# Kernel optimization log

Hardware: AMD Instinct MI355X
Metric: run time of the kernel (lower is better)

Reference implementation:

```python
import jax, jax.numpy as jnp
import numpy as np

NEG_SLOPE = 0.2
BN_EPS = 1e-5

def lrelu(x):
    return jnp.where(x >= 0, x, NEG_SLOPE * x)

def setup_inputs() -> dict:
    key = jax.random.key(0)
    ks = jax.random.split(key, 12)
    B, V, D = 256, 16, 512
    s = lambda fan_in: 1.0 / np.sqrt(fan_in)
    return {
        "F": jax.random.normal(ks[0], (B, V, D), dtype=jnp.float32),
        # Relation MLP: Linear(1024,512) x3 (stored as (in,out))
        "W1": jax.random.uniform(ks[1], (2 * D, D), jnp.float32, -s(2 * D), s(2 * D)),
        "b1": jax.random.uniform(ks[2], (D,), jnp.float32, -s(2 * D), s(2 * D)),
        "W2": jax.random.uniform(ks[3], (D, D), jnp.float32, -s(D), s(D)),
        "b2": jax.random.uniform(ks[4], (D,), jnp.float32, -s(D), s(D)),
        "W3": jax.random.uniform(ks[5], (D, D), jnp.float32, -s(D), s(D)),
        "b3": jax.random.uniform(ks[6], (D,), jnp.float32, -s(D), s(D)),
        # Fusion: Linear(1024,512) + BatchNorm1d(512)
        "Wf": jax.random.uniform(ks[7], (2 * D, D), jnp.float32, -s(2 * D), s(2 * D)),
        "bf": jax.random.uniform(ks[8], (D,), jnp.float32, -s(2 * D), s(2 * D)),
        "gamma": jnp.ones((D,), jnp.float32),
        "beta": jnp.zeros((D,), jnp.float32),
    }

def reference(F, W1, b1, W2, b2, W3, b3, Wf, bf, gamma, beta):
    B, V, D = F.shape
    # All-pairs broadcast + concat -> (B, V, V, 2D)
    F_i = jnp.broadcast_to(F[:, :, None, :], (B, V, V, D))
    F_j = jnp.broadcast_to(F[:, None, :, :], (B, V, V, D))
    M = jnp.concatenate([F_i, F_j], axis=-1)
    # 3-layer Relation MLP with LeakyReLU(0.2)
    h = lrelu(M @ W1 + b1)
    h = lrelu(h @ W2 + b2)
    h = lrelu(h @ W3 + b3)
    # Sum over neighbor axis (dim -2) -> (B, V, D)
    Msum = jnp.sum(h, axis=-2)
    # Fusion: concat, Linear, BatchNorm1d (training-mode batch stats), LeakyReLU
    X = jnp.concatenate([F, Msum], axis=-1).reshape(-1, 2 * D)  # (B*V, 2D)
    y = X @ Wf + bf
    mean = jnp.mean(y, axis=0)
    var = jnp.mean(jnp.square(y - mean), axis=0)  # biased var (torch BN)
    yn = (y - mean) * jax.lax.rsqrt(var + BN_EPS) * gamma + beta
    return lrelu(yn).reshape(B, V, D)
```

## Files before the change

kernel.cpp:

```cpp
#include <hip/hip_runtime.h>

using f32x4  = __attribute__((ext_vector_type(4))) float;
using bf16x8 = __attribute__((ext_vector_type(8))) __bf16;

static constexpr int DD = 512;
static constexpr int NTOK = 4096;

__device__ __forceinline__ float bf2f(unsigned short u) {
  unsigned int v = ((unsigned int)u) << 16;
  return __builtin_bit_cast(float, v);
}
__device__ __forceinline__ float bflo(unsigned int u) {
  return __builtin_bit_cast(float, u << 16);
}
__device__ __forceinline__ float bfhi(unsigned int u) {
  return __builtin_bit_cast(float, u & 0xffff0000u);
}
__device__ __forceinline__ unsigned short f2bf(float f) {
  unsigned int u = __builtin_bit_cast(unsigned int, f);
  unsigned int r = u + 0x7fffu + ((u >> 16) & 1u);
  return (unsigned short)(r >> 16);
}
__device__ __forceinline__ float lrelu(float v) { return v >= 0.f ? v : 0.2f * v; }


__global__ __launch_bounds__(256) void k_prep(const float* __restrict__ F,
                                              const float* __restrict__ W1,
                                              const float* __restrict__ W2,
                                              const float* __restrict__ W3,
                                              const float* __restrict__ Wf,
                                              unsigned short* __restrict__ XP,
                                              unsigned short* __restrict__ W1P,
                                              unsigned short* __restrict__ W2P,
                                              unsigned short* __restrict__ W3P,
                                              unsigned short* __restrict__ WfP,
                                              float* __restrict__ sums) {
  const int bid = blockIdx.x, tid = threadIdx.x;
  if (bid < 8192) {
    int idx = (bid << 8) + tid;
    int t = idx >> 9, c = idx & 511;
    XP[((t >> 4) * 32 + (c >> 5)) * 512 + ((c >> 3) & 3) * 128 + (t & 15) * 8 + (c & 7)] = f2bf(F[idx]);
  } else if (bid < 10240) {
    int idx = ((bid - 8192) << 8) + tid;
    int k = idx >> 10, n = idx & 1023;
    float v = W1[(n < 512 ? k : 512 + k) * 512 + (n & 511)];
    W1P[((n >> 4) * 16 + (k >> 5)) * 512 + ((k >> 3) & 3) * 128 + (n & 15) * 8 + (k & 7)] = f2bf(v);
  } else if (bid < 11264) {
    int idx = ((bid - 10240) << 8) + tid;
    int k = idx >> 9, n = idx & 511;
    int off = (((n >> 6) * 16 + (k >> 5)) * 4 + ((n >> 4) & 3)) * 512 + ((k >> 3) & 3) * 128 + (n & 15) * 8 + (k & 7);
    W2P[off] = f2bf(W2[idx]);
  } else if (bid < 12288) {
    int idx = ((bid - 11264) << 8) + tid;
    int k = idx >> 9, n = idx & 511;
    int off = (((n >> 6) * 16 + (k >> 5)) * 4 + ((n >> 4) & 3)) * 512 + ((k >> 3) & 3) * 128 + (n & 15) * 8 + (k & 7);
    W3P[off] = f2bf(W3[idx]);
  } else if (bid < 14336) {
    int idx = ((bid - 12288) << 8) + tid;
    int k = idx >> 9, n = idx & 511;
    WfP[((n >> 4) * 32 + (k >> 5)) * 512 + ((k >> 3) & 3) * 128 + (n & 15) * 8 + (k & 7)] = f2bf(Wf[idx]);
  } else {
    reinterpret_cast<float4*>(sums)[tid] = float4{0.f, 0.f, 0.f, 0.f};
  }
}

__global__ __launch_bounds__(512) void k_gemm_ac(const unsigned short* __restrict__ XP,
                                                 const unsigned short* __restrict__ W1P,
                                                 unsigned short* __restrict__ ACP) {
  const int tid = threadIdx.x, lane = tid & 63, wid = tid >> 6;
  const int wm = wid >> 2, wn = wid & 3;
  const int l15 = lane & 15;
  const int bx = blockIdx.x, by = blockIdx.y;

  f32x4 acc[2][4];
#pragma unroll
  for (int mt = 0; mt < 2; ++mt)
#pragma unroll
    for (int nt = 0; nt < 4; ++nt) acc[mt][nt] = f32x4{0.f, 0.f, 0.f, 0.f};

  bf16x8 ca[2], cb[4], na[2], nb[4];
  auto ldA = [&](bf16x8 (&d)[2], int ks) {
#pragma unroll
    for (int mt = 0; mt < 2; ++mt)
      d[mt] = *reinterpret_cast<const bf16x8*>(XP + (((bx * 4 + wm * 2 + mt) * 32 + ks) << 9) + lane * 8);
  };
  auto ldB = [&](bf16x8 (&d)[4], int ks) {
#pragma unroll
    for (int nt = 0; nt < 4; ++nt)
      d[nt] = *reinterpret_cast<const bf16x8*>(W1P + ((((by * 16 + wn * 4 + nt) * 16) + ks) << 9) + lane * 8);
  };

  ldA(ca, 0); ldB(cb, 0);
  for (int ks = 0; ks < 16; ++ks) {
    int kn = (ks + 1) & 15;
    ldA(na, kn); ldB(nb, kn);
    __builtin_amdgcn_s_setprio(1);
#pragma unroll
    for (int mt = 0; mt < 2; ++mt)
#pragma unroll
      for (int nt = 0; nt < 4; ++nt)
        acc[mt][nt] = __builtin_amdgcn_mfma_f32_16x16x32_bf16(ca[mt], cb[nt], acc[mt][nt], 0, 0, 0);
    __builtin_amdgcn_s_setprio(0);
#pragma unroll
    for (int q = 0; q < 2; ++q) ca[q] = na[q];
#pragma unroll
    for (int q = 0; q < 4; ++q) cb[q] = nb[q];
  }
#pragma unroll
  for (int mt = 0; mt < 2; ++mt)
#pragma unroll
    for (int nt = 0; nt < 4; ++nt) {
      int col = by * 256 + wn * 64 + nt * 16 + l15;
      int panel = bx * 4 + wm * 2 + mt;
#pragma unroll
      for (int r = 0; r < 4; ++r) {
        int rowi = (lane >> 4) * 4 + r;
        ACP[(panel * 32 + (col >> 5)) * 512 + ((col >> 3) & 3) * 128 + rowi * 8 + (col & 7)] = f2bf(acc[mt][nt][r]);
      }
    }
}

__global__ __launch_bounds__(1024) void k_relation(const unsigned short* __restrict__ ACP,
                                                   const unsigned short* __restrict__ W2P,
                                                   const unsigned short* __restrict__ W3P,
                                                   const float* __restrict__ b1,
                                                   const float* __restrict__ b2,
                                                   const float* __restrict__ b3,
                                                   unsigned short* __restrict__ XP) {
  __shared__ unsigned short lds[65536];
  char* ldsb = reinterpret_cast<char*>(lds);
  const int tid = threadIdx.x;
  const int b = blockIdx.x >> 1, half = blockIdx.x & 1;

  {
    const int r = tid >> 3;
    const int kh = (tid >> 2) & 1;
    const int kq = tid & 3;
    const int il = r >> 4, j = r & 15;
    const int rowA = half * 8 + il;
#pragma unroll
    for (int kk = 0; kk < 8; ++kk) {
      const int ks = kh * 8 + kk;
      const int c = ks * 32 + kq * 8;
      uint4 av = *reinterpret_cast<const uint4*>(ACP + ((b * 32 + ks) << 9) + kq * 128 + rowA * 8);
      uint4 cv = *reinterpret_cast<const uint4*>(ACP + ((b * 32 + 16 + ks) << 9) + kq * 128 + j * 8);
      float4 bv0 = *reinterpret_cast<const float4*>(b1 + c);
      float4 bv1 = *reinterpret_cast<const float4*>(b1 + c + 4);
      unsigned int au[4] = {av.x, av.y, av.z, av.w};
      unsigned int cu[4] = {cv.x, cv.y, cv.z, cv.w};
      float bb[8] = {bv0.x, bv0.y, bv0.z, bv0.w, bv1.x, bv1.y, bv1.z, bv1.w};
      unsigned int ou[4];
#pragma unroll
      for (int q = 0; q < 4; ++q) {
        float v0 = lrelu(bflo(au[q]) + bflo(cu[q]) + bb[2 * q]);
        float v1 = lrelu(bfhi(au[q]) + bfhi(cu[q]) + bb[2 * q + 1]);
        ou[q] = ((unsigned int)f2bf(v1) << 16) | (unsigned int)f2bf(v0);
      }
      uint4 o; o.x = ou[0]; o.y = ou[1]; o.z = ou[2]; o.w = ou[3];
      *reinterpret_cast<uint4*>(ldsb + ((r >> 4) * 16 + ks) * 1024 + kq * 256 + (r & 15) * 16) = o;
    }
  }
  __syncthreads();

  const int lane = tid & 63, wid = tid >> 6;
  const int l15 = lane & 15;
  const int fg = wid >> 1;
  const int rg = wid & 1;

  const unsigned short* w2base = W2P + (fg << 15) + lane * 8;
  const unsigned short* w3base = W3P + (fg << 15) + lane * 8;
  const char* lrd = ldsb + rg * 65536 + lane * 16;
  char* lwr = ldsb + rg * 65536 + fg * 2048 + ((lane >> 5) & 1) * 256 + ((lane >> 4) & 1) * 8 + l15 * 16;

  f32x4 acc[4][4];
  bf16x8 a[2][4], cb[4];

  auto layer = [&](const unsigned short* __restrict__ wb) {
#pragma unroll
    for (int mt = 0; mt < 4; ++mt)
#pragma unroll
      for (int nt = 0; nt < 4; ++nt) acc[mt][nt] = f32x4{0.f, 0.f, 0.f, 0.f};
#pragma unroll
    for (int mt = 0; mt < 4; ++mt)
      a[0][mt] = *reinterpret_cast<const bf16x8*>(wb + mt * 512);
#pragma unroll
    for (int ks = 0; ks < 16; ++ks) {
      const int cur = ks & 1, nxt = cur ^ 1;
      const int ksn = (ks + 1) & 15;
#pragma unroll
      for (int mt = 0; mt < 4; ++mt)
        a[nxt][mt] = *reinterpret_cast<const bf16x8*>(wb + ksn * 2048 + mt * 512);
#pragma unroll
      for (int nt = 0; nt < 4; ++nt)
        cb[nt] = *reinterpret_cast<const bf16x8*>(lrd + nt * 16384 + ks * 1024);
      __builtin_amdgcn_s_setprio(1);
#pragma unroll
      for (int mt = 0; mt < 4; ++mt)
#pragma unroll
        for (int nt = 0; nt < 4; ++nt)
          acc[mt][nt] = __builtin_amdgcn_mfma_f32_16x16x32_bf16(a[cur][mt], cb[nt], acc[mt][nt], 0, 0, 0);
      __builtin_amdgcn_s_setprio(0);
    }
  };

  auto store_h = [&](const float* __restrict__ bias) {
#pragma unroll
    for (int mt = 0; mt < 4; ++mt) {
      float4 bv = *reinterpret_cast<const float4*>(bias + fg * 64 + mt * 16 + ((lane >> 4) & 3) * 4);
#pragma unroll
      for (int nt = 0; nt < 4; ++nt) {
        unsigned int w0 = f2bf(lrelu(acc[mt][nt][0] + bv.x));
        unsigned int w1 = f2bf(lrelu(acc[mt][nt][1] + bv.y));
        unsigned int w2 = f2bf(lrelu(acc[mt][nt][2] + bv.z));
        unsigned int w3 = f2bf(lrelu(acc[mt][nt][3] + bv.w));
        uint2 val; val.x = (w1 << 16) | w0; val.y = (w3 << 16) | w2;
        *reinterpret_cast<uint2*>(lwr + nt * 16384 + (mt >> 1) * 1024 + (mt & 1) * 512) = val;
      }
    }
  };

  layer(w2base);
  __syncthreads();
  store_h(b2);
  __syncthreads();
  layer(w3base);
  __syncthreads();
  store_h(b3);
  __syncthreads();

  if (wid < 8) {
    const int t = wid;
    const int ks = lane >> 2, kq = lane & 3;
    const char* base = ldsb + (t * 16 + ks) * 1024 + kq * 256;
    float s[8] = {0.f, 0.f, 0.f, 0.f, 0.f, 0.f, 0.f, 0.f};
#pragma unroll
    for (int it = 0; it < 16; ++it) {
      int j = (it + lane + (lane >> 3)) & 15;
      uint4 v = *reinterpret_cast<const uint4*>(base + j * 16);
      s[0] += bflo(v.x); s[1] += bfhi(v.x);
      s[2] += bflo(v.y); s[3] += bfhi(v.y);
      s[4] += bflo(v.z); s[5] += bfhi(v.z);
      s[6] += bflo(v.w); s[7] += bfhi(v.w);
    }
    uint4 o;
    o.x = ((unsigned int)f2bf(s[1]) << 16) | f2bf(s[0]);
    o.y = ((unsigned int)f2bf(s[3]) << 16) | f2bf(s[2]);
    o.z = ((unsigned int)f2bf(s[5]) << 16) | f2bf(s[4]);
    o.w = ((unsigned int)f2bf(s[7]) << 16) | f2bf(s[6]);
    int tg15 = half * 8 + t;
    *reinterpret_cast<uint4*>(XP + ((b * 32 + 16 + ks) << 9) + kq * 128 + tg15 * 8) = o;
  }
}

__global__ __launch_bounds__(512) void k_fusion(const unsigned short* __restrict__ XP,
                                                const unsigned short* __restrict__ WfP,
                                                const float* __restrict__ bfv,
                                                float* __restrict__ y,
                                                float* __restrict__ sums,
                                                float* __restrict__ sumsq) {
  const int tid = threadIdx.x, lane = tid & 63, wid = tid >> 6;
  const int wm = wid >> 2, wn = wid & 3;
  const int l15 = lane & 15;
  const int bx = blockIdx.x, by = blockIdx.y;
  const int rowbase = bx * 64 + wm * 32;
  const int colbase = by * 128 + wn * 32;

  f32x4 acc[2][2];
#pragma unroll
  for (int mt = 0; mt < 2; ++mt)
#pragma unroll
    for (int nt = 0; nt < 2; ++nt) acc[mt][nt] = f32x4{0.f, 0.f, 0.f, 0.f};

  bf16x8 ca[2], cb[2], na[2], nb[2];
  auto ldA = [&](bf16x8 (&d)[2], int ks) {
#pragma unroll
    for (int mt = 0; mt < 2; ++mt)
      d[mt] = *reinterpret_cast<const bf16x8*>(XP + (((bx * 4 + wm * 2 + mt) * 32 + ks) << 9) + lane * 8);
  };
  auto ldB = [&](bf16x8 (&d)[2], int ks) {
#pragma unroll
    for (int nt = 0; nt < 2; ++nt)
      d[nt] = *reinterpret_cast<const bf16x8*>(WfP + (((by * 8 + wn * 2 + nt) * 32 + ks) << 9) + lane * 8);
  };

  ldA(ca, 0); ldB(cb, 0);
  for (int ks = 0; ks < 32; ++ks) {
    int kn = (ks + 1) & 31;
    ldA(na, kn); ldB(nb, kn);
    __builtin_amdgcn_s_setprio(1);
#pragma unroll
    for (int mt = 0; mt < 2; ++mt)
#pragma unroll
      for (int nt = 0; nt < 2; ++nt)
        acc[mt][nt] = __builtin_amdgcn_mfma_f32_16x16x32_bf16(ca[mt], cb[nt], acc[mt][nt], 0, 0, 0);
    __builtin_amdgcn_s_setprio(0);
#pragma unroll
    for (int q = 0; q < 2; ++q) { ca[q] = na[q]; cb[q] = nb[q]; }
  }

  float s[2] = {0.f, 0.f}, q2[2] = {0.f, 0.f};
#pragma unroll
  for (int nt = 0; nt < 2; ++nt) {
    int col = colbase + nt * 16 + l15;
    float bias = bfv[col];
#pragma unroll
    for (int mt = 0; mt < 2; ++mt)
#pragma unroll
      for (int r = 0; r < 4; ++r) {
        int row = rowbase + mt * 16 + (lane >> 4) * 4 + r;
        float v = acc[mt][nt][r] + bias;
        y[row * DD + col] = v;
        s[nt] += v; q2[nt] += v * v;
      }
  }
#pragma unroll
  for (int nt = 0; nt < 2; ++nt) {
    s[nt] += __shfl_xor(s[nt], 16);  s[nt] += __shfl_xor(s[nt], 32);
    q2[nt] += __shfl_xor(q2[nt], 16); q2[nt] += __shfl_xor(q2[nt], 32);
    if (lane < 16) {
      int col = colbase + nt * 16 + l15;
      atomicAdd(&sums[col], s[nt]);
      atomicAdd(&sumsq[col], q2[nt]);
    }
  }
}

__global__ __launch_bounds__(256) void k_bnapply(const float* __restrict__ y,
                                                 const float* __restrict__ sums,
                                                 const float* __restrict__ sumsq,
                                                 const float* __restrict__ gamma,
                                                 const float* __restrict__ beta,
                                                 float* __restrict__ out) {
  int idx = blockIdx.x * 256 + threadIdx.x;
  if (idx >= NTOK * DD) return;
  int c = idx & 511;
  float mean = sums[c] * (1.0f / 4096.0f);
  float var = sumsq[c] * (1.0f / 4096.0f) - mean * mean;
  float rstd = rsqrtf(var + 1e-5f);
  float v = (y[idx] - mean) * rstd * gamma[c] + beta[c];
  out[idx] = lrelu(v);
}

extern "C" void kernel_launch(void* const* d_in, const int* in_sizes, int n_in,
                              void* d_out, int out_size, void* d_ws, size_t ws_size,
                              hipStream_t stream) {
  const float* F   = (const float*)d_in[0];
  const float* W1  = (const float*)d_in[1];
  const float* b1  = (const float*)d_in[2];
  const float* W2  = (const float*)d_in[3];
  const float* b2  = (const float*)d_in[4];
  const float* W3  = (const float*)d_in[5];
  const float* b3  = (const float*)d_in[6];
  const float* Wf  = (const float*)d_in[7];
  const float* bfv = (const float*)d_in[8];
  const float* gamma = (const float*)d_in[9];
  const float* beta  = (const float*)d_in[10];
  float* out = (float*)d_out;

  char* ws = (char*)d_ws;
  unsigned short* XP  = (unsigned short*)(ws);
  unsigned short* ACP = (unsigned short*)(ws + (8u << 20));
  unsigned short* W1P = (unsigned short*)(ws + (16u << 20));
  unsigned short* W2P = (unsigned short*)(ws + (17u << 20));
  unsigned short* W3P = (unsigned short*)(ws + (17u << 20) + (512u << 10));
  unsigned short* WfP = (unsigned short*)(ws + (18u << 20));
  float* y            = (float*)(ws + (19u << 20));
  float* sums         = (float*)(ws + (27u << 20));
  float* sumsq        = sums + 512;

  k_prep<<<14337, 256, 0, stream>>>(F, W1, W2, W3, Wf, XP, W1P, W2P, W3P, WfP, sums);
  k_gemm_ac<<<dim3(64, 4), 512, 0, stream>>>(XP, W1P, ACP);
  k_relation<<<512, 1024, 0, stream>>>(ACP, W2P, W3P, b1, b2, b3, XP);
  k_fusion<<<dim3(64, 4), 512, 0, stream>>>(XP, WfP, bfv, y, sums, sumsq);
  k_bnapply<<<(NTOK * DD + 255) / 256, 256, 0, stream>>>(y, sums, sumsq, gamma, beta, out);
}
```

Baseline: 124.3 us.

## Switch relation MLP to 32x32x16 MFMA with matching weight and LDS layouts

Replaces the 4x4 grid of 16x16x32 bf16 MFMAs in the relation kernel with a 2x2 grid of 32x32x16 MFMAs per wave. The W2/W3 packing, the LDS layout for the hidden activations, the layer-1 staging and the neighbor-sum readout are all re-indexed to fit the new fragment shapes. The k-loop is now a rolled, software-pipelined ping-pong over 32 k-steps, and launch_bounds gains a minimum-occupancy hint. The aim is fewer fragment loads per FLOP and fewer MFMA issues, at the cost of new LDS bank-conflict patterns and a possible register-pressure cap from the occupancy hint.

```diff
diff --git a/kernel.cpp b/kernel.cpp
--- a/kernel.cpp
+++ b/kernel.cpp
@@ -1,6 +1,7 @@
 #include <hip/hip_runtime.h>
 
 using f32x4  = __attribute__((ext_vector_type(4))) float;
+using f32x16 = __attribute__((ext_vector_type(16))) float;
 using bf16x8 = __attribute__((ext_vector_type(8))) __bf16;
 
 static constexpr int DD = 512;
@@ -48,12 +49,14 @@
   } else if (bid < 11264) {
     int idx = ((bid - 10240) << 8) + tid;
     int k = idx >> 9, n = idx & 511;
-    int off = (((n >> 6) * 16 + (k >> 5)) * 4 + ((n >> 4) & 3)) * 512 + ((k >> 3) & 3) * 128 + (n & 15) * 8 + (k & 7);
+    int off = (((n >> 6) * 32 + (k >> 4)) * 2 + ((n >> 5) & 1)) * 512 +
+              ((k >> 3) & 1) * 256 + (n & 31) * 8 + (k & 7);
     W2P[off] = f2bf(W2[idx]);
   } else if (bid < 12288) {
     int idx = ((bid - 11264) << 8) + tid;
     int k = idx >> 9, n = idx & 511;
-    int off = (((n >> 6) * 16 + (k >> 5)) * 4 + ((n >> 4) & 3)) * 512 + ((k >> 3) & 3) * 128 + (n & 15) * 8 + (k & 7);
+    int off = (((n >> 6) * 32 + (k >> 4)) * 2 + ((n >> 5) & 1)) * 512 +
+              ((k >> 3) & 1) * 256 + (n & 31) * 8 + (k & 7);
     W3P[off] = f2bf(W3[idx]);
   } else if (bid < 14336) {
     int idx = ((bid - 12288) << 8) + tid;
@@ -120,32 +123,31 @@
     }
 }
 
-__global__ __launch_bounds__(1024) void k_relation(const unsigned short* __restrict__ ACP,
-                                                   const unsigned short* __restrict__ W2P,
-                                                   const unsigned short* __restrict__ W3P,
-                                                   const float* __restrict__ b1,
-                                                   const float* __restrict__ b2,
-                                                   const float* __restrict__ b3,
-                                                   unsigned short* __restrict__ XP) {
+__global__ __launch_bounds__(1024, 4) void k_relation(const unsigned short* __restrict__ ACP,
+                                                      const unsigned short* __restrict__ W2P,
+                                                      const unsigned short* __restrict__ W3P,
+                                                      const float* __restrict__ b1,
+                                                      const float* __restrict__ b2,
+                                                      const float* __restrict__ b3,
+                                                      unsigned short* __restrict__ XP) {
   __shared__ unsigned short lds[65536];
   char* ldsb = reinterpret_cast<char*>(lds);
   const int tid = threadIdx.x;
   const int b = blockIdx.x >> 1, half = blockIdx.x & 1;
 
   {
-    const int r = tid >> 3;
-    const int kh = (tid >> 2) & 1;
-    const int kq = tid & 3;
+    const int c8b = (tid >> 3) & 7;
+    const int r = ((tid >> 6) << 3) | (tid & 7);
     const int il = r >> 4, j = r & 15;
     const int rowA = half * 8 + il;
-#pragma unroll
-    for (int kk = 0; kk < 8; ++kk) {
-      const int ks = kh * 8 + kk;
-      const int c = ks * 32 + kq * 8;
-      uint4 av = *reinterpret_cast<const uint4*>(ACP + ((b * 32 + ks) << 9) + kq * 128 + rowA * 8);
-      uint4 cv = *reinterpret_cast<const uint4*>(ACP + ((b * 32 + 16 + ks) << 9) + kq * 128 + j * 8);
-      float4 bv0 = *reinterpret_cast<const float4*>(b1 + c);
-      float4 bv1 = *reinterpret_cast<const float4*>(b1 + c + 4);
+    const int rt = r >> 5, r31 = r & 31;
+#pragma unroll
+    for (int it = 0; it < 8; ++it) {
+      const int c8 = c8b + it * 8;
+      uint4 av = *reinterpret_cast<const uint4*>(ACP + ((b * 32 + (c8 >> 2)) << 9) + (c8 & 3) * 128 + rowA * 8);
+      uint4 cv = *reinterpret_cast<const uint4*>(ACP + ((b * 32 + 16 + (c8 >> 2)) << 9) + (c8 & 3) * 128 + j * 8);
+      float4 bv0 = *reinterpret_cast<const float4*>(b1 + c8 * 8);
+      float4 bv1 = *reinterpret_cast<const float4*>(b1 + c8 * 8 + 4);
       unsigned int au[4] = {av.x, av.y, av.z, av.w};
       unsigned int cu[4] = {cv.x, cv.y, cv.z, cv.w};
       float bb[8] = {bv0.x, bv0.y, bv0.z, bv0.w, bv1.x, bv1.y, bv1.z, bv1.w};
@@ -157,66 +159,78 @@
         ou[q] = ((unsigned int)f2bf(v1) << 16) | (unsigned int)f2bf(v0);
       }
       uint4 o; o.x = ou[0]; o.y = ou[1]; o.z = ou[2]; o.w = ou[3];
-      *reinterpret_cast<uint4*>(ldsb + ((r >> 4) * 16 + ks) * 1024 + kq * 256 + (r & 15) * 16) = o;
+      *reinterpret_cast<uint4*>(ldsb + (rt * 32 + (c8 >> 1)) * 1024 + (c8 & 1) * 512 + r31 * 16) = o;
     }
   }
   __syncthreads();
 
   const int lane = tid & 63, wid = tid >> 6;
-  const int l15 = lane & 15;
+  const int r31 = lane & 31, h = lane >> 5;
   const int fg = wid >> 1;
   const int rg = wid & 1;
 
   const unsigned short* w2base = W2P + (fg << 15) + lane * 8;
   const unsigned short* w3base = W3P + (fg << 15) + lane * 8;
-  const char* lrd = ldsb + rg * 65536 + lane * 16;
-  char* lwr = ldsb + rg * 65536 + fg * 2048 + ((lane >> 5) & 1) * 256 + ((lane >> 4) & 1) * 8 + l15 * 16;
-
-  f32x4 acc[4][4];
-  bf16x8 a[2][4], cb[4];
+  const unsigned short* lrd = lds + (rg * 2) * 32 * 512 + lane * 8;
+
+  f32x16 acc[2][2];
+  bf16x8 aA[2], aB[2], bA[2], bB[2];
+
+  auto ldA_ = [&](bf16x8 (&d)[2], const unsigned short* __restrict__ wb, int ks) {
+    d[0] = *reinterpret_cast<const bf16x8*>(wb + ks * 1024);
+    d[1] = *reinterpret_cast<const bf16x8*>(wb + ks * 1024 + 512);
+  };
+  auto ldB_ = [&](bf16x8 (&d)[2], int ks) {
+    d[0] = *reinterpret_cast<const bf16x8*>(lrd + ks * 512);
+    d[1] = *reinterpret_cast<const bf16x8*>(lrd + 32 * 512 + ks * 512);
+  };
 
   auto layer = [&](const unsigned short* __restrict__ wb) {
 #pragma unroll
-    for (int mt = 0; mt < 4; ++mt)
-#pragma unroll
-      for (int nt = 0; nt < 4; ++nt) acc[mt][nt] = f32x4{0.f, 0.f, 0.f, 0.f};
-#pragma unroll
-    for (int mt = 0; mt < 4; ++mt)
-      a[0][mt] = *reinterpret_cast<const bf16x8*>(wb + mt * 512);
-#pragma unroll
-    for (int ks = 0; ks < 16; ++ks) {
-      const int cur = ks & 1, nxt = cur ^ 1;
-      const int ksn = (ks + 1) & 15;
-#pragma unroll
-      for (int mt = 0; mt < 4; ++mt)
-        a[nxt][mt] = *reinterpret_cast<const bf16x8*>(wb + ksn * 2048 + mt * 512);
-#pragma unroll
-      for (int nt = 0; nt < 4; ++nt)
-        cb[nt] = *reinterpret_cast<const bf16x8*>(lrd + nt * 16384 + ks * 1024);
+    for (int mt = 0; mt < 2; ++mt)
+#pragma unroll
+      for (int nt = 0; nt < 2; ++nt)
+#pragma unroll
+        for (int e = 0; e < 16; ++e) acc[mt][nt][e] = 0.f;
+    ldA_(aA, wb, 0); ldB_(bA, 0);
+#pragma unroll 1
+    for (int ks = 0; ks < 32; ks += 2) {
+      ldA_(aB, wb, ks + 1); ldB_(bB, ks + 1);
       __builtin_amdgcn_s_setprio(1);
-#pragma unroll
-      for (int mt = 0; mt < 4; ++mt)
-#pragma unroll
-        for (int nt = 0; nt < 4; ++nt)
-          acc[mt][nt] = __builtin_amdgcn_mfma_f32_16x16x32_bf16(a[cur][mt], cb[nt], acc[mt][nt], 0, 0, 0);
+      acc[0][0] = __builtin_amdgcn_mfma_f32_32x32x16_bf16(aA[0], bA[0], acc[0][0], 0, 0, 0);
+      acc[0][1] = __builtin_amdgcn_mfma_f32_32x32x16_bf16(aA[0], bA[1], acc[0][1], 0, 0, 0);
+      acc[1][0] = __builtin_amdgcn_mfma_f32_32x32x16_bf16(aA[1], bA[0], acc[1][0], 0, 0, 0);
+      acc[1][1] = __builtin_amdgcn_mfma_f32_32x32x16_bf16(aA[1], bA[1], acc[1][1], 0, 0, 0);
       __builtin_amdgcn_s_setprio(0);
+      const int ksn = (ks + 2) & 31;
+      ldA_(aA, wb, ksn); ldB_(bA, ksn);
+      __builtin_amdgcn_s_setprio(1);
+      acc[0][0] = __builtin_amdgcn_mfma_f32_32x32x16_bf16(aB[0], bB[0], acc[0][0], 0, 0, 0);
+      acc[0][1] = __builtin_amdgcn_mfma_f32_32x32x16_bf16(aB[0], bB[1], acc[0][1], 0, 0, 0);
+      acc[1][0] = __builtin_amdgcn_mfma_f32_32x32x16_bf16(aB[1], bB[0], acc[1][0], 0, 0, 0);
+      acc[1][1] = __builtin_amdgcn_mfma_f32_32x32x16_bf16(aB[1], bB[1], acc[1][1], 0, 0, 0);
+      __builtin_amdgcn_s_setprio(0);
     }
   };
 
   auto store_h = [&](const float* __restrict__ bias) {
 #pragma unroll
-    for (int mt = 0; mt < 4; ++mt) {
-      float4 bv = *reinterpret_cast<const float4*>(bias + fg * 64 + mt * 16 + ((lane >> 4) & 3) * 4);
-#pragma unroll
-      for (int nt = 0; nt < 4; ++nt) {
-        unsigned int w0 = f2bf(lrelu(acc[mt][nt][0] + bv.x));
-        unsigned int w1 = f2bf(lrelu(acc[mt][nt][1] + bv.y));
-        unsigned int w2 = f2bf(lrelu(acc[mt][nt][2] + bv.z));
-        unsigned int w3 = f2bf(lrelu(acc[mt][nt][3] + bv.w));
-        uint2 val; val.x = (w1 << 16) | w0; val.y = (w3 << 16) | w2;
-        *reinterpret_cast<uint2*>(lwr + nt * 16384 + (mt >> 1) * 1024 + (mt & 1) * 512) = val;
+    for (int mt = 0; mt < 2; ++mt)
+#pragma unroll
+      for (int g = 0; g < 4; ++g) {
+        float4 bv = *reinterpret_cast<const float4*>(bias + fg * 64 + mt * 32 + g * 8 + h * 4);
+        const int ks16 = fg * 4 + mt * 2 + (g >> 1);
+        const int kh = g & 1;
+#pragma unroll
+        for (int nt = 0; nt < 2; ++nt) {
+          unsigned int w0 = f2bf(lrelu(acc[mt][nt][4 * g + 0] + bv.x));
+          unsigned int w1 = f2bf(lrelu(acc[mt][nt][4 * g + 1] + bv.y));
+          unsigned int w2 = f2bf(lrelu(acc[mt][nt][4 * g + 2] + bv.z));
+          unsigned int w3 = f2bf(lrelu(acc[mt][nt][4 * g + 3] + bv.w));
+          uint2 val; val.x = (w1 << 16) | w0; val.y = (w3 << 16) | w2;
+          *reinterpret_cast<uint2*>(ldsb + ((rg * 2 + nt) * 32 + ks16) * 1024 + kh * 512 + r31 * 16 + h * 8) = val;
+        }
       }
-    }
   };
 
   layer(w2base);
@@ -230,25 +244,25 @@
 
   if (wid < 8) {
     const int t = wid;
-    const int ks = lane >> 2, kq = lane & 3;
-    const char* base = ldsb + (t * 16 + ks) * 1024 + kq * 256;
+    const int o = lane;
+    const char* base = ldsb + ((t >> 1) * 32 + (o >> 1)) * 1024 + (o & 1) * 512 + (t & 1) * 256;
     float s[8] = {0.f, 0.f, 0.f, 0.f, 0.f, 0.f, 0.f, 0.f};
 #pragma unroll
     for (int it = 0; it < 16; ++it) {
-      int j = (it + lane + (lane >> 3)) & 15;
+      int j = (it + o) & 15;
       uint4 v = *reinterpret_cast<const uint4*>(base + j * 16);
       s[0] += bflo(v.x); s[1] += bfhi(v.x);
       s[2] += bflo(v.y); s[3] += bfhi(v.y);
       s[4] += bflo(v.z); s[5] += bfhi(v.z);
       s[6] += bflo(v.w); s[7] += bfhi(v.w);
     }
-    uint4 o;
-    o.x = ((unsigned int)f2bf(s[1]) << 16) | f2bf(s[0]);
-    o.y = ((unsigned int)f2bf(s[3]) << 16) | f2bf(s[2]);
-    o.z = ((unsigned int)f2bf(s[5]) << 16) | f2bf(s[4]);
-    o.w = ((unsigned int)f2bf(s[7]) << 16) | f2bf(s[6]);
+    uint4 o4;
+    o4.x = ((unsigned int)f2bf(s[1]) << 16) | f2bf(s[0]);
+    o4.y = ((unsigned int)f2bf(s[3]) << 16) | f2bf(s[2]);
+    o4.z = ((unsigned int)f2bf(s[5]) << 16) | f2bf(s[4]);
+    o4.w = ((unsigned int)f2bf(s[7]) << 16) | f2bf(s[6]);
     int tg15 = half * 8 + t;
-    *reinterpret_cast<uint4*>(XP + ((b * 32 + 16 + ks) << 9) + kq * 128 + tg15 * 8) = o;
+    *reinterpret_cast<uint4*>(XP + ((b * 32 + 16 + (o >> 2)) << 9) + (o & 3) * 128 + tg15 * 8) = o4;
   }
 }
 
```

Measured after the change: 126.7 us. No clear change (+1.9%).
